# Performance work log

Hardware: AMD Instinct MI355X
Metric: run time of the kernel (lower is better)

Reference implementation:

```python
import jax, jax.numpy as jnp
import numpy as np

D_MODEL = 1024
NUM_EXPERTS = 8
TOP_K = 2
B, S = 1, 2048


def setup_inputs() -> dict:
    key = jax.random.key(0)
    ks = jax.random.split(key, 8)
    sd = 1.0 / np.sqrt(D_MODEL)
    x = jax.random.normal(ks[0], (B, S, D_MODEL), dtype=jnp.float32)
    gate_w = jax.random.normal(ks[1], (D_MODEL, NUM_EXPERTS), dtype=jnp.float32) * sd
    gate_b = jnp.zeros((NUM_EXPERTS,), dtype=jnp.float32)
    w1 = jax.random.normal(ks[2], (NUM_EXPERTS, D_MODEL, 8 * D_MODEL), dtype=jnp.float32) * sd
    b1 = jnp.zeros((NUM_EXPERTS, 8 * D_MODEL), dtype=jnp.float32)
    w2 = jax.random.normal(ks[3], (NUM_EXPERTS, 4 * D_MODEL, D_MODEL), dtype=jnp.float32) * (1.0 / np.sqrt(4 * D_MODEL))
    b2 = jnp.zeros((NUM_EXPERTS, D_MODEL), dtype=jnp.float32)
    return {"x": x, "gate_w": gate_w, "gate_b": gate_b, "w1": w1, "b1": b1, "w2": w2, "b2": b2}


def reference(x, gate_w, gate_b, w1, b1, w2, b2):
    # Gating: top-k logits, softmax over the selected k
    gate_logits = jnp.einsum('bsd,de->bse', x, gate_w) + gate_b          # [B,S,E]
    weights, indices = jax.lax.top_k(gate_logits, TOP_K)                  # [B,S,K]
    weights = jax.nn.softmax(weights, axis=-1)

    # Dense all-expert compute (matches original masked-sum math; dropout in eval)
    h = jnp.einsum('bsd,edh->ebsh', x, w1) + b1[:, None, None, :]         # [E,B,S,8D]
    xh, gh = jnp.split(h, 2, axis=-1)                                     # each [E,B,S,4D]
    act = jax.nn.silu(gh) * xh
    out_e = jnp.einsum('ebsf,efd->ebsd', act, w2) + b2[:, None, None, :]  # [E,B,S,D]

    # Combine: gather the top-k expert outputs per token and weight-sum
    out_e = jnp.transpose(out_e, (1, 2, 0, 3))                            # [B,S,E,D]
    sel = jnp.take_along_axis(out_e, indices[..., None], axis=2)          # [B,S,K,D]
    return jnp.sum(sel * weights[..., None], axis=2)                      # [B,S,D]
```

## Files before the change

kernel.cpp:

```cpp
#include <hip/hip_runtime.h>
#include <hip/hip_bf16.h>

#define S 2048
#define D 1024
#define NE 8
#define HF 4096
#define HH 8192
#define BK 32
#define ACT_ROWS 4224
#define MAXRB 40

typedef __attribute__((ext_vector_type(8))) __bf16 bf16x8;
typedef __attribute__((ext_vector_type(4))) float f32x4;

__device__ __forceinline__ unsigned cvtpk(float lo, float hi) {
  unsigned r;
  asm("v_cvt_pk_bf16_f32 %0, %1, %2" : "=v"(r) : "v"(lo), "v"(hi));
  return r;
}
__device__ __forceinline__ unsigned bf16b(float f) {
  unsigned b = __float_as_uint(f);
  return (b + 0x7fffu + ((b >> 16) & 1u)) >> 16;
}
__device__ __forceinline__ void gll16(const ushort* g, ushort* l) {
  __builtin_amdgcn_global_load_lds(
      (const __attribute__((address_space(1))) void*)g,
      (__attribute__((address_space(3))) void*)l, 16, 0, 0);
}

__global__ __launch_bounds__(256) void convert_x(const float* __restrict__ x,
                                                 ushort* __restrict__ xb) {
  const int idx = blockIdx.x * 256 + threadIdx.x;
  const float4* src = (const float4*)x;
  float4 a = src[idx * 2], b = src[idx * 2 + 1];
  uint4 w = {cvtpk(a.x, a.y), cvtpk(a.z, a.w), cvtpk(b.x, b.y), cvtpk(b.z, b.w)};
  ((uint4*)xb)[idx] = w;
}

__global__ __launch_bounds__(256) void transpose_convert(const float* __restrict__ src,
                                                         ushort* __restrict__ dst,
                                                         int R, int C) {
  const int e = blockIdx.z;
  const int n0 = blockIdx.x * 64;
  const int k0 = blockIdx.y * 64;
  const float* Sp = src + (size_t)e * R * C;
  ushort* Dp = dst + (size_t)e * R * C;
  __shared__ unsigned T[64][33];
  const int t = threadIdx.x;
  const int kp = t >> 4;
  const int nn = (t & 15) * 4;
#pragma unroll
  for (int j = 0; j < 2; ++j) {
    const int ka = k0 + 2 * kp + 32 * j;
    float4 a = *(const float4*)(Sp + (size_t)ka * C + n0 + nn);
    float4 b = *(const float4*)(Sp + (size_t)(ka + 1) * C + n0 + nn);
    T[nn + 0][kp + 16 * j] = cvtpk(a.x, b.x);
    T[nn + 1][kp + 16 * j] = cvtpk(a.y, b.y);
    T[nn + 2][kp + 16 * j] = cvtpk(a.z, b.z);
    T[nn + 3][kp + 16 * j] = cvtpk(a.w, b.w);
  }
  __syncthreads();
  const int n = t >> 2;
  const int kq = (t & 3) * 8;
  uint4 v0 = *(const uint4*)&T[n][kq];
  uint4 v1 = *(const uint4*)&T[n][kq + 4];
  uint4* out = (uint4*)(Dp + (size_t)(n0 + n) * R + k0 + kq * 2);
  out[0] = v0;
  out[1] = v1;
}

__global__ void gate_kernel(const float* __restrict__ x, const float* __restrict__ gw,
                            const float* __restrict__ gb,
                            int* __restrict__ mi0, int* __restrict__ mi1,
                            float* __restrict__ mw0, float* __restrict__ mw1) {
  const int t = blockIdx.x;
  const int l = threadIdx.x;
  const float* xr = x + (size_t)t * D;
  float acc[NE];
#pragma unroll
  for (int e = 0; e < NE; ++e) acc[e] = 0.f;
  for (int d = l; d < D; d += 64) {
    float xv = xr[d];
    const float* g = gw + (size_t)d * NE;
#pragma unroll
    for (int e = 0; e < NE; ++e) acc[e] += xv * g[e];
  }
#pragma unroll
  for (int e = 0; e < NE; ++e) {
    float v = acc[e];
#pragma unroll
    for (int off = 32; off > 0; off >>= 1) v += __shfl_xor(v, off);
    acc[e] = v;
  }
  if (l == 0) {
    float lg[NE];
#pragma unroll
    for (int e = 0; e < NE; ++e) lg[e] = acc[e] + gb[e];
    int i0 = 0; float m0 = lg[0];
#pragma unroll
    for (int e = 1; e < NE; ++e) if (lg[e] > m0) { m0 = lg[e]; i0 = e; }
    int i1 = -1; float m1 = -3.4e38f;
#pragma unroll
    for (int e = 0; e < NE; ++e) if (e != i0 && lg[e] > m1) { m1 = lg[e]; i1 = e; }
    float p = __expf(m1 - m0);
    float inv = 1.f / (1.f + p);
    mi0[t] = i0; mi1[t] = i1;
    mw0[t] = inv; mw1[t] = p * inv;
  }
}

__global__ __launch_bounds__(1024) void route_kernel(
    const int* __restrict__ mi0, const int* __restrict__ mi1,
    int* __restrict__ counts, int* __restrict__ basep, int* __restrict__ list_tok,
    int* __restrict__ mr0, int* __restrict__ mr1,
    int* __restrict__ rb_e, int* __restrict__ rb_row0, int* __restrict__ rb_n) {
  __shared__ int cnt[NE];
  __shared__ int cur[NE];
  const int t = threadIdx.x;
  if (t < NE) cnt[t] = 0;
  __syncthreads();
  const int e0a = mi0[t], e1a = mi1[t];
  const int e0b = mi0[t + 1024], e1b = mi1[t + 1024];
  atomicAdd(&cnt[e0a], 1); atomicAdd(&cnt[e1a], 1);
  atomicAdd(&cnt[e0b], 1); atomicAdd(&cnt[e1b], 1);
  __syncthreads();
  if (t == 0) {
    int s = 0;
#pragma unroll
    for (int e = 0; e < NE; ++e) { basep[e] = s; cur[e] = s; s += cnt[e]; }
    basep[NE] = s;
    int nrb = 0;
    for (int e = 0; e < NE; ++e)
      for (int r0 = 0; r0 < cnt[e]; r0 += 128) {
        rb_e[nrb] = e; rb_row0[nrb] = r0; ++nrb;
      }
    *rb_n = nrb;
  }
  if (t < NE) counts[t] = cnt[t];
  __syncthreads();
  int r;
  r = atomicAdd(&cur[e0a], 1); list_tok[r] = t; mr0[t] = r;
  r = atomicAdd(&cur[e1a], 1); list_tok[r] = t; mr1[t] = r;
  r = atomicAdd(&cur[e0b], 1); list_tok[r] = t + 1024; mr0[t + 1024] = r;
  r = atomicAdd(&cur[e1b], 1); list_tok[r] = t + 1024; mr1[t + 1024] = r;
}

__global__ __launch_bounds__(256) void gemm1_kernel(
    const ushort* __restrict__ xb, const ushort* __restrict__ w1t,
    const float* __restrict__ b1, const int* __restrict__ counts,
    const int* __restrict__ basep, const int* __restrict__ list_tok,
    const int* __restrict__ rb_e, const int* __restrict__ rb_row0,
    const int* __restrict__ rb_n, ushort* __restrict__ act_buf) {
  const int rb = blockIdx.y;
  if (rb >= *rb_n) return;
  const int e = rb_e[rb];
  const int row0 = rb_row0[rb];
  const int cnt = counts[e];
  const int jt = blockIdx.x * 64;
  const ushort* __restrict__ W = w1t + (size_t)e * D * HH;
  const int gbase = basep[e];

  __shared__ ushort As[2][128][BK];
  __shared__ ushort Bs[2][128][BK];

  const int tid = threadIdx.x;
  const int w = tid >> 6;
  const int i = tid & 63;

  const int rA0 = w * 32 + (i >> 2);
  const int rA1 = rA0 + 16;
  int s0 = row0 + rA0; if (s0 >= cnt) s0 = cnt - 1;
  int s1 = row0 + rA1; if (s1 >= cnt) s1 = cnt - 1;
  const ushort* pa0 = xb + (size_t)list_tok[gbase + s0] * D + (i & 3) * 8;
  const ushort* pa1 = xb + (size_t)list_tok[gbase + s1] * D + (i & 3) * 8;
  const ushort* pb0 = W + ((size_t)(rA0 >> 6) * HF + jt + (rA0 & 63)) * D + (i & 3) * 8;
  const ushort* pb1 = W + ((size_t)(rA1 >> 6) * HF + jt + (rA1 & 63)) * D + (i & 3) * 8;

  const int wm = (w >> 1) * 64;
  const int wn = (w & 1) * 32;
  const int lr = i & 15;
  const int kg = i >> 4;

  f32x4 acc[2][4][2] = {};

  gll16(pa0, &As[0][w * 32][0]);
  gll16(pa1, &As[0][w * 32 + 16][0]);
  gll16(pb0, &Bs[0][w * 32][0]);
  gll16(pb1, &Bs[0][w * 32 + 16][0]);
  __syncthreads();

  int cur = 0;
#pragma unroll 1
  for (int it = 0; it < D / BK; ++it) {
    if (it + 1 < D / BK) {
      const int ko = (it + 1) * BK;
      gll16(pa0 + ko, &As[cur ^ 1][w * 32][0]);
      gll16(pa1 + ko, &As[cur ^ 1][w * 32 + 16][0]);
      gll16(pb0 + ko, &Bs[cur ^ 1][w * 32][0]);
      gll16(pb1 + ko, &Bs[cur ^ 1][w * 32 + 16][0]);
    }
    bf16x8 af[4], bfr[2][2];
#pragma unroll
    for (int mi = 0; mi < 4; ++mi)
      af[mi] = *(const bf16x8*)&As[cur][wm + mi * 16 + lr][kg * 8];
#pragma unroll
    for (int h = 0; h < 2; ++h)
#pragma unroll
      for (int ni = 0; ni < 2; ++ni)
        bfr[h][ni] = *(const bf16x8*)&Bs[cur][h * 64 + wn + ni * 16 + lr][kg * 8];
#pragma unroll
    for (int h = 0; h < 2; ++h)
#pragma unroll
      for (int mi = 0; mi < 4; ++mi)
#pragma unroll
        for (int ni = 0; ni < 2; ++ni)
          acc[h][mi][ni] = __builtin_amdgcn_mfma_f32_16x16x32_bf16(af[mi], bfr[h][ni],
                                                                   acc[h][mi][ni], 0, 0, 0);
    __syncthreads();
    cur ^= 1;
  }

#pragma unroll
  for (int mi = 0; mi < 4; ++mi)
#pragma unroll
    for (int ni = 0; ni < 2; ++ni) {
      const int c = jt + wn + ni * 16 + lr;
      const float bx = b1[(size_t)e * HH + c];
      const float bg = b1[(size_t)e * HH + HF + c];
      f32x4 vx = acc[0][mi][ni];
      f32x4 vg = acc[1][mi][ni];
#pragma unroll
      for (int q = 0; q < 4; ++q) {
        const int slot = row0 + wm + mi * 16 + kg * 4 + q;
        if (slot < cnt) {
          float xv = vx[q] + bx;
          float g = vg[q] + bg;
          float a = g / (1.f + __expf(-g)) * xv;
          act_buf[(size_t)(gbase + slot) * HF + c] = (ushort)bf16b(a);
        }
      }
    }
}

__global__ __launch_bounds__(256) void gemm2_kernel(
    const ushort* __restrict__ act_buf, const ushort* __restrict__ w2t,
    const int* __restrict__ counts, const int* __restrict__ basep,
    const int* __restrict__ rb_e, const int* __restrict__ rb_row0,
    const int* __restrict__ rb_n, float* __restrict__ oe) {
  const int rb = blockIdx.y;
  if (rb >= *rb_n) return;
  const int e = rb_e[rb];
  const int row0 = rb_row0[rb];
  const int cnt = counts[e];
  const int split = blockIdx.z;
  const int jt = blockIdx.x * 128;
  const ushort* __restrict__ W = w2t + (size_t)e * HF * D;
  const int gbase = basep[e];

  __shared__ ushort As[2][128][BK];
  __shared__ ushort Bs[2][128][BK];

  const int tid = threadIdx.x;
  const int w = tid >> 6;
  const int i = tid & 63;

  const int r0 = w * 32 + (i >> 2);
  const size_t kbase = (size_t)split * (HF / 2);
  const ushort* pa0 = act_buf + (size_t)(gbase + row0 + r0) * HF + kbase + (i & 3) * 8;
  const ushort* pa1 = pa0 + (size_t)16 * HF;
  const ushort* pb0 = W + (size_t)(jt + r0) * HF + kbase + (i & 3) * 8;
  const ushort* pb1 = pb0 + (size_t)16 * HF;

  const int wm = (w >> 1) * 64;
  const int wn = (w & 1) * 64;
  const int lr = i & 15;
  const int kg = i >> 4;

  f32x4 acc[4][4] = {};

  gll16(pa0, &As[0][w * 32][0]);
  gll16(pa1, &As[0][w * 32 + 16][0]);
  gll16(pb0, &Bs[0][w * 32][0]);
  gll16(pb1, &Bs[0][w * 32 + 16][0]);
  __syncthreads();

  int cur = 0;
#pragma unroll 1
  for (int it = 0; it < (HF / 2) / BK; ++it) {
    if (it + 1 < (HF / 2) / BK) {
      const int ko = (it + 1) * BK;
      gll16(pa0 + ko, &As[cur ^ 1][w * 32][0]);
      gll16(pa1 + ko, &As[cur ^ 1][w * 32 + 16][0]);
      gll16(pb0 + ko, &Bs[cur ^ 1][w * 32][0]);
      gll16(pb1 + ko, &Bs[cur ^ 1][w * 32 + 16][0]);
    }
    bf16x8 af[4], bfr[4];
#pragma unroll
    for (int mi = 0; mi < 4; ++mi)
      af[mi] = *(const bf16x8*)&As[cur][wm + mi * 16 + lr][kg * 8];
#pragma unroll
    for (int ni = 0; ni < 4; ++ni)
      bfr[ni] = *(const bf16x8*)&Bs[cur][wn + ni * 16 + lr][kg * 8];
#pragma unroll
    for (int mi = 0; mi < 4; ++mi)
#pragma unroll
      for (int ni = 0; ni < 4; ++ni)
        acc[mi][ni] = __builtin_amdgcn_mfma_f32_16x16x32_bf16(af[mi], bfr[ni],
                                                              acc[mi][ni], 0, 0, 0);
    __syncthreads();
    cur ^= 1;
  }

#pragma unroll
  for (int mi = 0; mi < 4; ++mi)
#pragma unroll
    for (int ni = 0; ni < 4; ++ni) {
      f32x4 v = acc[mi][ni];
#pragma unroll
      for (int q = 0; q < 4; ++q) {
        const int slot = row0 + wm + mi * 16 + kg * 4 + q;
        if (slot < cnt)
          oe[((size_t)split * ACT_ROWS + gbase + slot) * D + jt + wn + ni * 16 + lr] = v[q];
      }
    }
}

__global__ void combine_kernel(const float* __restrict__ oe,
                               const int* __restrict__ mr0, const int* __restrict__ mr1,
                               const float* __restrict__ mw0, const float* __restrict__ mw1,
                               const int* __restrict__ mi0, const int* __restrict__ mi1,
                               const float* __restrict__ b2, float* __restrict__ out) {
  const int t = blockIdx.x;
  const int l = threadIdx.x;
  const float w0 = mw0[t], w1 = mw1[t];
  const float4* p00 = (const float4*)(oe + (size_t)mr0[t] * D);
  const float4* p01 = (const float4*)(oe + ((size_t)ACT_ROWS + mr0[t]) * D);
  const float4* p10 = (const float4*)(oe + (size_t)mr1[t] * D);
  const float4* p11 = (const float4*)(oe + ((size_t)ACT_ROWS + mr1[t]) * D);
  const float4* c0 = (const float4*)(b2 + (size_t)mi0[t] * D);
  const float4* c1 = (const float4*)(b2 + (size_t)mi1[t] * D);
  float4 A0 = p00[l], A1 = p01[l], B0 = p10[l], B1 = p11[l], C = c0[l], E2 = c1[l];
  float4 r;
  r.x = w0 * (A0.x + A1.x + C.x) + w1 * (B0.x + B1.x + E2.x);
  r.y = w0 * (A0.y + A1.y + C.y) + w1 * (B0.y + B1.y + E2.y);
  r.z = w0 * (A0.z + A1.z + C.z) + w1 * (B0.z + B1.z + E2.z);
  r.w = w0 * (A0.w + A1.w + C.w) + w1 * (B0.w + B1.w + E2.w);
  ((float4*)(out + (size_t)t * D))[l] = r;
}

extern "C" void kernel_launch(void* const* d_in, const int* in_sizes, int n_in,
                              void* d_out, int out_size, void* d_ws, size_t ws_size,
                              hipStream_t stream) {
  const float* x  = (const float*)d_in[0];
  const float* gw = (const float*)d_in[1];
  const float* gb = (const float*)d_in[2];
  const float* w1 = (const float*)d_in[3];
  const float* b1 = (const float*)d_in[4];
  const float* w2 = (const float*)d_in[5];
  const float* b2 = (const float*)d_in[6];
  float* out = (float*)d_out;

  char* ws = (char*)d_ws;
  int*   counts   = (int*)(ws + 0);
  int*   basep    = (int*)(ws + 64);
  int*   rb_n     = (int*)(ws + 128);
  int*   rb_e     = (int*)(ws + 192);
  int*   rb_row0  = (int*)(ws + 384);
  int*   mi0      = (int*)(ws + 1024);
  int*   mi1      = (int*)(ws + 1024 + 1 * 8192);
  int*   mr0      = (int*)(ws + 1024 + 2 * 8192);
  int*   mr1      = (int*)(ws + 1024 + 3 * 8192);
  float* mw0      = (float*)(ws + 1024 + 4 * 8192);
  float* mw1      = (float*)(ws + 1024 + 5 * 8192);
  int*   list_tok = (int*)(ws + 1024 + 6 * 8192);
  ushort* xb      = (ushort*)(ws + 66560);
  ushort* act_buf = (ushort*)(ws + 4260864);
  float*  oe      = (float*)(ws + 38863872);
  ushort* w1t     = (ushort*)(ws + 73466880);
  ushort* w2t     = (ushort*)(ws + 207684608);

  convert_x<<<(S * D) / (256 * 8), 256, 0, stream>>>(x, xb);
  transpose_convert<<<dim3(HH / 64, D / 64, NE), 256, 0, stream>>>(w1, w1t, D, HH);
  transpose_convert<<<dim3(D / 64, HF / 64, NE), 256, 0, stream>>>(w2, w2t, HF, D);
  gate_kernel<<<S, 64, 0, stream>>>(x, gw, gb, mi0, mi1, mw0, mw1);
  route_kernel<<<1, 1024, 0, stream>>>(mi0, mi1, counts, basep, list_tok, mr0, mr1,
                                       rb_e, rb_row0, rb_n);
  gemm1_kernel<<<dim3(64, MAXRB), 256, 0, stream>>>(xb, w1t, b1, counts, basep, list_tok,
                                                    rb_e, rb_row0, rb_n, act_buf);
  gemm2_kernel<<<dim3(8, MAXRB, 2), 256, 0, stream>>>(act_buf, w2t, counts, basep,
                                                      rb_e, rb_row0, rb_n, oe);
  combine_kernel<<<S, 256, 0, stream>>>(oe, mr0, mr1, mw0, mw1, mi0, mi1, b2, out);
}
```

Baseline: 326.6 us.

## Fuse x conversion into gating, scatter-add gemm2 output directly, split-K by four

The bf16 conversion of x moves into a 256-thread gate kernel that also computes the logits, which removes the separate convert_x launch. The per-expert oe buffer and the combine kernel are removed: out is pre-initialised with the weighted biases, and gemm2 atomically adds weighted partial results straight into the token rows. gemm2 split-K goes from 2 to 4 to get more blocks in flight. In exchange, float atomics are issued per element, the summation order becomes nondeterministic, and atomic traffic to the same rows grows with more splits.

```diff
diff --git a/kernel.cpp b/kernel.cpp
--- a/kernel.cpp
+++ b/kernel.cpp
@@ -26,15 +26,6 @@
   __builtin_amdgcn_global_load_lds(
       (const __attribute__((address_space(1))) void*)g,
       (__attribute__((address_space(3))) void*)l, 16, 0, 0);
-}
-
-__global__ __launch_bounds__(256) void convert_x(const float* __restrict__ x,
-                                                 ushort* __restrict__ xb) {
-  const int idx = blockIdx.x * 256 + threadIdx.x;
-  const float4* src = (const float4*)x;
-  float4 a = src[idx * 2], b = src[idx * 2 + 1];
-  uint4 w = {cvtpk(a.x, a.y), cvtpk(a.z, a.w), cvtpk(b.x, b.y), cvtpk(b.z, b.w)};
-  ((uint4*)xb)[idx] = w;
 }
 
 __global__ __launch_bounds__(256) void transpose_convert(const float* __restrict__ src,
@@ -69,22 +60,26 @@
   out[1] = v1;
 }
 
-__global__ void gate_kernel(const float* __restrict__ x, const float* __restrict__ gw,
-                            const float* __restrict__ gb,
-                            int* __restrict__ mi0, int* __restrict__ mi1,
-                            float* __restrict__ mw0, float* __restrict__ mw1) {
+__global__ __launch_bounds__(256) void gate_kernel(
+    const float* __restrict__ x, const float* __restrict__ gw,
+    const float* __restrict__ gb, ushort* __restrict__ xb,
+    int* __restrict__ mi0, int* __restrict__ mi1,
+    float* __restrict__ mw0, float* __restrict__ mw1) {
   const int t = blockIdx.x;
   const int l = threadIdx.x;
-  const float* xr = x + (size_t)t * D;
+  const float4 xv = ((const float4*)(x + (size_t)t * D))[l];
+  uint2 wv = {cvtpk(xv.x, xv.y), cvtpk(xv.z, xv.w)};
+  ((uint2*)(xb + (size_t)t * D))[l] = wv;
+
+  float xa[4] = {xv.x, xv.y, xv.z, xv.w};
   float acc[NE];
 #pragma unroll
   for (int e = 0; e < NE; ++e) acc[e] = 0.f;
-  for (int d = l; d < D; d += 64) {
-    float xv = xr[d];
-    const float* g = gw + (size_t)d * NE;
-#pragma unroll
-    for (int e = 0; e < NE; ++e) acc[e] += xv * g[e];
-  }
+  const float* g0 = gw + (size_t)(4 * l) * NE;
+#pragma unroll
+  for (int j = 0; j < 4; ++j)
+#pragma unroll
+    for (int e = 0; e < NE; ++e) acc[e] += xa[j] * g0[j * NE + e];
 #pragma unroll
   for (int e = 0; e < NE; ++e) {
     float v = acc[e];
@@ -92,10 +87,18 @@
     for (int off = 32; off > 0; off >>= 1) v += __shfl_xor(v, off);
     acc[e] = v;
   }
+  __shared__ float sm[4][NE];
+  const int wid = l >> 6;
+  if ((l & 63) == 0) {
+#pragma unroll
+    for (int e = 0; e < NE; ++e) sm[wid][e] = acc[e];
+  }
+  __syncthreads();
   if (l == 0) {
     float lg[NE];
 #pragma unroll
-    for (int e = 0; e < NE; ++e) lg[e] = acc[e] + gb[e];
+    for (int e = 0; e < NE; ++e)
+      lg[e] = sm[0][e] + sm[1][e] + sm[2][e] + sm[3][e] + gb[e];
     int i0 = 0; float m0 = lg[0];
 #pragma unroll
     for (int e = 1; e < NE; ++e) if (lg[e] > m0) { m0 = lg[e]; i0 = e; }
@@ -111,8 +114,9 @@
 
 __global__ __launch_bounds__(1024) void route_kernel(
     const int* __restrict__ mi0, const int* __restrict__ mi1,
+    const float* __restrict__ mw0, const float* __restrict__ mw1,
     int* __restrict__ counts, int* __restrict__ basep, int* __restrict__ list_tok,
-    int* __restrict__ mr0, int* __restrict__ mr1,
+    float* __restrict__ list_w,
     int* __restrict__ rb_e, int* __restrict__ rb_row0, int* __restrict__ rb_n) {
   __shared__ int cnt[NE];
   __shared__ int cur[NE];
@@ -139,10 +143,23 @@
   if (t < NE) counts[t] = cnt[t];
   __syncthreads();
   int r;
-  r = atomicAdd(&cur[e0a], 1); list_tok[r] = t; mr0[t] = r;
-  r = atomicAdd(&cur[e1a], 1); list_tok[r] = t; mr1[t] = r;
-  r = atomicAdd(&cur[e0b], 1); list_tok[r] = t + 1024; mr0[t + 1024] = r;
-  r = atomicAdd(&cur[e1b], 1); list_tok[r] = t + 1024; mr1[t + 1024] = r;
+  r = atomicAdd(&cur[e0a], 1); list_tok[r] = t;        list_w[r] = mw0[t];
+  r = atomicAdd(&cur[e1a], 1); list_tok[r] = t;        list_w[r] = mw1[t];
+  r = atomicAdd(&cur[e0b], 1); list_tok[r] = t + 1024; list_w[r] = mw0[t + 1024];
+  r = atomicAdd(&cur[e1b], 1); list_tok[r] = t + 1024; list_w[r] = mw1[t + 1024];
+}
+
+__global__ __launch_bounds__(256) void init_out(
+    const float* __restrict__ b2, const int* __restrict__ mi0, const int* __restrict__ mi1,
+    const float* __restrict__ mw0, const float* __restrict__ mw1, float* __restrict__ out) {
+  const int t = blockIdx.x;
+  const int l = threadIdx.x;
+  const float w0 = mw0[t], w1 = mw1[t];
+  float4 a = ((const float4*)(b2 + (size_t)mi0[t] * D))[l];
+  float4 b = ((const float4*)(b2 + (size_t)mi1[t] * D))[l];
+  float4 r = {w0 * a.x + w1 * b.x, w0 * a.y + w1 * b.y,
+              w0 * a.z + w1 * b.z, w0 * a.w + w1 * b.w};
+  ((float4*)(out + (size_t)t * D))[l] = r;
 }
 
 __global__ __launch_bounds__(256) void gemm1_kernel(
@@ -245,8 +262,9 @@
 __global__ __launch_bounds__(256) void gemm2_kernel(
     const ushort* __restrict__ act_buf, const ushort* __restrict__ w2t,
     const int* __restrict__ counts, const int* __restrict__ basep,
+    const int* __restrict__ list_tok, const float* __restrict__ list_w,
     const int* __restrict__ rb_e, const int* __restrict__ rb_row0,
-    const int* __restrict__ rb_n, float* __restrict__ oe) {
+    const int* __restrict__ rb_n, float* __restrict__ out) {
   const int rb = blockIdx.y;
   if (rb >= *rb_n) return;
   const int e = rb_e[rb];
@@ -265,7 +283,7 @@
   const int i = tid & 63;
 
   const int r0 = w * 32 + (i >> 2);
-  const size_t kbase = (size_t)split * (HF / 2);
+  const size_t kbase = (size_t)split * (HF / 4);
   const ushort* pa0 = act_buf + (size_t)(gbase + row0 + r0) * HF + kbase + (i & 3) * 8;
   const ushort* pa1 = pa0 + (size_t)16 * HF;
   const ushort* pb0 = W + (size_t)(jt + r0) * HF + kbase + (i & 3) * 8;
@@ -286,8 +304,8 @@
 
   int cur = 0;
 #pragma unroll 1
-  for (int it = 0; it < (HF / 2) / BK; ++it) {
-    if (it + 1 < (HF / 2) / BK) {
+  for (int it = 0; it < (HF / 4) / BK; ++it) {
+    if (it + 1 < (HF / 4) / BK) {
       const int ko = (it + 1) * BK;
       gll16(pa0 + ko, &As[cur ^ 1][w * 32][0]);
       gll16(pa1 + ko, &As[cur ^ 1][w * 32 + 16][0]);
@@ -312,40 +330,21 @@
   }
 
 #pragma unroll
-  for (int mi = 0; mi < 4; ++mi)
-#pragma unroll
-    for (int ni = 0; ni < 4; ++ni) {
-      f32x4 v = acc[mi][ni];
-#pragma unroll
-      for (int q = 0; q < 4; ++q) {
-        const int slot = row0 + wm + mi * 16 + kg * 4 + q;
-        if (slot < cnt)
-          oe[((size_t)split * ACT_ROWS + gbase + slot) * D + jt + wn + ni * 16 + lr] = v[q];
+  for (int mi = 0; mi < 4; ++mi) {
+    const int slotb = row0 + wm + mi * 16 + kg * 4;
+#pragma unroll
+    for (int q = 0; q < 4; ++q) {
+      const int slot = slotb + q;
+      if (slot < cnt) {
+        const int tok = list_tok[gbase + slot];
+        const float wgt = list_w[gbase + slot];
+        float* orow = out + (size_t)tok * D + jt + wn + lr;
+#pragma unroll
+        for (int ni = 0; ni < 4; ++ni)
+          atomicAdd(orow + ni * 16, wgt * acc[mi][ni][q]);
       }
     }
-}
-
-__global__ void combine_kernel(const float* __restrict__ oe,
-                               const int* __restrict__ mr0, const int* __restrict__ mr1,
-                               const float* __restrict__ mw0, const float* __restrict__ mw1,
-                               const int* __restrict__ mi0, const int* __restrict__ mi1,
-                               const float* __restrict__ b2, float* __restrict__ out) {
-  const int t = blockIdx.x;
-  const int l = threadIdx.x;
-  const float w0 = mw0[t], w1 = mw1[t];
-  const float4* p00 = (const float4*)(oe + (size_t)mr0[t] * D);
-  const float4* p01 = (const float4*)(oe + ((size_t)ACT_ROWS + mr0[t]) * D);
-  const float4* p10 = (const float4*)(oe + (size_t)mr1[t] * D);
-  const float4* p11 = (const float4*)(oe + ((size_t)ACT_ROWS + mr1[t]) * D);
-  const float4* c0 = (const float4*)(b2 + (size_t)mi0[t] * D);
-  const float4* c1 = (const float4*)(b2 + (size_t)mi1[t] * D);
-  float4 A0 = p00[l], A1 = p01[l], B0 = p10[l], B1 = p11[l], C = c0[l], E2 = c1[l];
-  float4 r;
-  r.x = w0 * (A0.x + A1.x + C.x) + w1 * (B0.x + B1.x + E2.x);
-  r.y = w0 * (A0.y + A1.y + C.y) + w1 * (B0.y + B1.y + E2.y);
-  r.z = w0 * (A0.z + A1.z + C.z) + w1 * (B0.z + B1.z + E2.z);
-  r.w = w0 * (A0.w + A1.w + C.w) + w1 * (B0.w + B1.w + E2.w);
-  ((float4*)(out + (size_t)t * D))[l] = r;
+  }
 }
 
 extern "C" void kernel_launch(void* const* d_in, const int* in_sizes, int n_in,
@@ -367,27 +366,25 @@
   int*   rb_e     = (int*)(ws + 192);
   int*   rb_row0  = (int*)(ws + 384);
   int*   mi0      = (int*)(ws + 1024);
-  int*   mi1      = (int*)(ws + 1024 + 1 * 8192);
-  int*   mr0      = (int*)(ws + 1024 + 2 * 8192);
-  int*   mr1      = (int*)(ws + 1024 + 3 * 8192);
-  float* mw0      = (float*)(ws + 1024 + 4 * 8192);
-  float* mw1      = (float*)(ws + 1024 + 5 * 8192);
-  int*   list_tok = (int*)(ws + 1024 + 6 * 8192);
+  int*   mi1      = (int*)(ws + 9216);
+  float* mw0      = (float*)(ws + 17408);
+  float* mw1      = (float*)(ws + 25600);
+  int*   list_tok = (int*)(ws + 33792);
+  float* list_w   = (float*)(ws + 50176);
   ushort* xb      = (ushort*)(ws + 66560);
   ushort* act_buf = (ushort*)(ws + 4260864);
-  float*  oe      = (float*)(ws + 38863872);
-  ushort* w1t     = (ushort*)(ws + 73466880);
-  ushort* w2t     = (ushort*)(ws + 207684608);
-
-  convert_x<<<(S * D) / (256 * 8), 256, 0, stream>>>(x, xb);
+  ushort* w1t     = (ushort*)(ws + 38863872);
+  ushort* w2t     = (ushort*)(ws + 173081600);
+
   transpose_convert<<<dim3(HH / 64, D / 64, NE), 256, 0, stream>>>(w1, w1t, D, HH);
   transpose_convert<<<dim3(D / 64, HF / 64, NE), 256, 0, stream>>>(w2, w2t, HF, D);
-  gate_kernel<<<S, 64, 0, stream>>>(x, gw, gb, mi0, mi1, mw0, mw1);
-  route_kernel<<<1, 1024, 0, stream>>>(mi0, mi1, counts, basep, list_tok, mr0, mr1,
-                                       rb_e, rb_row0, rb_n);
+  gate_kernel<<<S, 256, 0, stream>>>(x, gw, gb, xb, mi0, mi1, mw0, mw1);
+  route_kernel<<<1, 1024, 0, stream>>>(mi0, mi1, mw0, mw1, counts, basep, list_tok,
+                                       list_w, rb_e, rb_row0, rb_n);
+  init_out<<<S, 256, 0, stream>>>(b2, mi0, mi1, mw0, mw1, out);
   gemm1_kernel<<<dim3(64, MAXRB), 256, 0, stream>>>(xb, w1t, b1, counts, basep, list_tok,
                                                     rb_e, rb_row0, rb_n, act_buf);
-  gemm2_kernel<<<dim3(8, MAXRB, 2), 256, 0, stream>>>(act_buf, w2t, counts, basep,
-                                                      rb_e, rb_row0, rb_n, oe);
-  combine_kernel<<<S, 256, 0, stream>>>(oe, mr0, mr1, mw0, mw1, mi0, mi1, b2, out);
-}
+  gemm2_kernel<<<dim3(8, MAXRB, 4), 256, 0, stream>>>(act_buf, w2t, counts, basep,
+                                                      list_tok, list_w,
+                                                      rb_e, rb_row0, rb_n, out);
+}
```

After: 352.1 us. 1.08x slower.
